# Performance work log

Measured on AMD Instinct MI355X. Metric: run time of the kernel, lower is better.

The kernel has to match this reference:

```python
import jax, jax.numpy as jnp
import numpy as np

N_NODES = 50000
N_EDGES = 500000
D_IN = 128
D_HID = 128
D_OUT = 128
N_GRAPHS = 1024


def gcn_conv(x, W, b, row, col, n_nodes):
    # x: [N, d_in] -> [N, d_out]; PyG GCNConv with add_self_loops + symmetric norm
    h = x @ W  # [N, d_out]
    loops = jnp.arange(n_nodes, dtype=row.dtype)
    r = jnp.concatenate([row, loops])  # source
    c = jnp.concatenate([col, loops])  # target
    deg = jax.ops.segment_sum(jnp.ones(r.shape[0], dtype=x.dtype), c, num_segments=n_nodes)
    dinv = jnp.where(deg > 0, jax.lax.rsqrt(jnp.maximum(deg, 1.0)), 0.0)
    norm = dinv[r] * dinv[c]  # [E+N]
    msg = h[r] * norm[:, None]  # gather + scale
    out = jax.ops.segment_sum(msg, c, num_segments=n_nodes)  # scatter-add at targets
    return out + b


def setup_inputs() -> dict:
    key = jax.random.key(0)
    ks = jax.random.split(key, 10)
    x = jax.random.normal(ks[0], (N_NODES, D_IN), dtype=jnp.float32)
    edge_index = jax.random.randint(ks[1], (2, N_EDGES), 0, N_NODES, dtype=jnp.int64)
    batch = jnp.sort(jax.random.randint(ks[2], (N_NODES,), 0, N_GRAPHS, dtype=jnp.int64))
    s1 = 1.0 / np.sqrt(D_IN)
    s2 = 1.0 / np.sqrt(D_HID)
    W1 = jax.random.uniform(ks[3], (D_IN, D_HID), jnp.float32, -s1, s1)
    b1 = jnp.zeros((D_HID,), jnp.float32)
    W2 = jax.random.uniform(ks[4], (D_HID, D_HID), jnp.float32, -s2, s2)
    b2 = jnp.zeros((D_HID,), jnp.float32)
    Wf = jax.random.uniform(ks[5], (D_HID, D_OUT), jnp.float32, -s2, s2)
    bf = jax.random.uniform(ks[6], (D_OUT,), jnp.float32, -s2, s2)
    return {"x": x, "edge_index": edge_index, "batch": batch,
            "W1": W1, "b1": b1, "W2": W2, "b2": b2, "Wf": Wf, "bf": bf}


def reference(x, edge_index, batch, W1, b1, W2, b2, Wf, bf):
    n = x.shape[0]
    row, col = edge_index[0], edge_index[1]
    h = jax.nn.relu(gcn_conv(x, W1, b1, row, col, n))
    h = jax.nn.relu(gcn_conv(h, W2, b2, row, col, n))
    # global_mean_pool over graph ids
    sums = jax.ops.segment_sum(h, batch, num_segments=N_GRAPHS)  # [G, d]
    cnts = jax.ops.segment_sum(jnp.ones((n,), h.dtype), batch, num_segments=N_GRAPHS)
    pooled = sums / jnp.maximum(cnts, 1.0)[:, None]
    return pooled @ Wf + bf  # [G, D_OUT]
```

## Files before the change

### kernel.cpp

```cpp
#include <hip/hip_runtime.h>
#include <hip/hip_bf16.h>


#define D 128

typedef __attribute__((ext_vector_type(8))) short short8;
typedef __attribute__((ext_vector_type(4))) float f32x4;

__device__ __forceinline__ int swz(int row, int kbyte) {
    return row * 256 + (kbyte ^ ((row & 7) << 4));
}

__global__ void k_zero(int4* __restrict__ p, int n4) {
    int i = blockIdx.x * blockDim.x + threadIdx.x;
    if (i < n4) p[i] = make_int4(0, 0, 0, 0);
}

__global__ void k_deg(const int* __restrict__ col, int* __restrict__ cnt, int E) {
    int e = blockIdx.x * blockDim.x + threadIdx.x;
    if (e < E) atomicAdd(&cnt[col[e]], 1);
}

__global__ __launch_bounds__(256) void k_scan_partial(const int* __restrict__ cnt,
                                                      int* __restrict__ partial, int n) {
    int t = threadIdx.x;
    int base = blockIdx.x * 1024 + t * 4;
    int s = 0;
#pragma unroll
    for (int j = 0; j < 4; ++j) {
        int i = base + j;
        if (i < n) s += cnt[i];
    }
#pragma unroll
    for (int o = 32; o > 0; o >>= 1) s += __shfl_down(s, o, 64);
    __shared__ int ws[4];
    if ((t & 63) == 0) ws[t >> 6] = s;
    __syncthreads();
    if (t == 0) partial[blockIdx.x] = ws[0] + ws[1] + ws[2] + ws[3];
}

__global__ void k_scan_mid(int* __restrict__ partial, int nb,
                           int* __restrict__ offs, int n) {
    if (threadIdx.x == 0 && blockIdx.x == 0) {
        int run = 0;
        for (int i = 0; i < nb; ++i) { int v = partial[i]; partial[i] = run; run += v; }
        offs[n] = run;
    }
}

__global__ __launch_bounds__(256) void k_scan_final(const int* __restrict__ cnt,
                                                    const int* __restrict__ pprefix,
                                                    int* __restrict__ offs,
                                                    int* __restrict__ cursor,
                                                    float* __restrict__ dinv, int n) {
    int t = threadIdx.x;
    int lane = t & 63;
    int base = blockIdx.x * 1024 + t * 4;
    int v[4];
    int s = 0;
#pragma unroll
    for (int j = 0; j < 4; ++j) {
        int i = base + j;
        v[j] = (i < n) ? cnt[i] : 0;
        s += v[j];
    }
    int inc = s;
#pragma unroll
    for (int o = 1; o < 64; o <<= 1) {
        int u = __shfl_up(inc, o, 64);
        if (lane >= o) inc += u;
    }
    __shared__ int wsum[4];
    if (lane == 63) wsum[t >> 6] = inc;
    __syncthreads();
    int woff = 0;
    int w = t >> 6;
    for (int k = 0; k < w; ++k) woff += wsum[k];
    int excl = woff + (inc - s) + pprefix[blockIdx.x];
#pragma unroll
    for (int j = 0; j < 4; ++j) {
        int i = base + j;
        if (i < n) {
            offs[i] = excl;
            cursor[i] = excl;
            dinv[i] = 1.0f / sqrtf((float)(v[j] + 1));
        }
        excl += v[j];
    }
}

__global__ void k_fill(const int* __restrict__ ei, int* __restrict__ cursor,
                       int* __restrict__ csr, int E) {
    int e = blockIdx.x * blockDim.x + threadIdx.x;
    if (e < E) {
        int r = ei[e];
        int c = ei[E + e];
        int pos = atomicAdd(&cursor[c], 1);
        csr[pos] = r;
    }
}

__global__ __launch_bounds__(256) void k_wcvt(const float* __restrict__ W1,
                                              const float* __restrict__ W2,
                                              ushort* __restrict__ h1, ushort* __restrict__ l1,
                                              ushort* __restrict__ h2, ushort* __restrict__ l2) {
    int b = blockIdx.x;
    const float* W = (b < 8) ? W1 : W2;
    ushort* Wh = (b < 8) ? h1 : h2;
    ushort* Wl = (b < 8) ? l1 : l2;
    int t = (b & 7) * 256 + threadIdx.x;
    int nrow = t >> 4;
    int kc = t & 15;
    uint hw[8], lw[8];
#pragma unroll
    for (int j = 0; j < 8; ++j) {
        float f = W[(kc * 8 + j) * D + nrow];
        uint ub = __float_as_uint(f);
        uint hb = ub & 0xffff0000u;
        float r = f - __uint_as_float(hb);
        hw[j] = hb >> 16;
        lw[j] = __float_as_uint(r) >> 16;
    }
    uint4 vh = make_uint4(hw[0] | (hw[1] << 16), hw[2] | (hw[3] << 16),
                          hw[4] | (hw[5] << 16), hw[6] | (hw[7] << 16));
    uint4 vl = make_uint4(lw[0] | (lw[1] << 16), lw[2] | (lw[3] << 16),
                          lw[4] | (lw[5] << 16), lw[6] | (lw[7] << 16));
    *(uint4*)&Wh[nrow * D + kc * 8] = vh;
    *(uint4*)&Wl[nrow * D + kc * 8] = vl;
}

#define TM 64
template <bool ASLICED>
__global__ __launch_bounds__(256) void k_gemm(const float* __restrict__ A,
                                              const ushort* __restrict__ Bt_hi,
                                              const ushort* __restrict__ Bt_lo,
                                              const float* __restrict__ dinv,
                                              float* __restrict__ C, int n) {
    extern __shared__ char lds[];
    char* Bh = lds;
    char* Bl = lds + 32 * 1024;

    int tid = threadIdx.x;
    int wave = tid >> 6, lane = tid & 63;
    int li = lane & 15, lg = lane >> 4;
    int row0 = blockIdx.x * TM;
    int grow = row0 + wave * 16 + li;
    bool valid = grow < n;

    float4 a[4][2];
#pragma unroll
    for (int ks = 0; ks < 4; ++ks) {
        int k0 = ks * 32 + lg * 8;
        if (valid) {
            const float4* p;
            if (ASLICED)
                p = (const float4*)(A + ((size_t)(k0 >> 4) * n + grow) * 16 + (k0 & 15));
            else
                p = (const float4*)(A + (size_t)grow * D + k0);
            a[ks][0] = p[0];
            a[ks][1] = p[1];
        } else {
            a[ks][0] = make_float4(0.f, 0.f, 0.f, 0.f);
            a[ks][1] = make_float4(0.f, 0.f, 0.f, 0.f);
        }
    }

#pragma unroll
    for (int it = tid; it < 2048; it += 256) {
        int r = it >> 4, kc = it & 15;
        uint4 vh = *(const uint4*)(Bt_hi + r * D + kc * 8);
        uint4 vl = *(const uint4*)(Bt_lo + r * D + kc * 8);
        *(uint4*)(Bh + swz(r, kc * 16)) = vh;
        *(uint4*)(Bl + swz(r, kc * 16)) = vl;
    }
    __syncthreads();

    short8 ah[4], al[4];
#pragma unroll
    for (int ks = 0; ks < 4; ++ks) {
        float f[8] = {a[ks][0].x, a[ks][0].y, a[ks][0].z, a[ks][0].w,
                      a[ks][1].x, a[ks][1].y, a[ks][1].z, a[ks][1].w};
#pragma unroll
        for (int j = 0; j < 8; ++j) {
            uint ub = __float_as_uint(f[j]);
            uint hb = ub & 0xffff0000u;
            float r = f[j] - __uint_as_float(hb);
            ah[ks][j] = (short)(hb >> 16);
            al[ks][j] = (short)(__float_as_uint(r) >> 16);
        }
    }

    f32x4 acc[8];
#pragma unroll
    for (int i = 0; i < 8; ++i) acc[i] = (f32x4){0.f, 0.f, 0.f, 0.f};

#pragma unroll
    for (int ks = 0; ks < 4; ++ks) {
        int kb = ks * 64 + lg * 16;
#pragma unroll
        for (int nt = 0; nt < 8; ++nt) {
            short8 bh = *(const short8*)(Bh + swz(nt * 16 + li, kb));
            short8 bl = *(const short8*)(Bl + swz(nt * 16 + li, kb));
            acc[nt] = __builtin_amdgcn_mfma_f32_16x16x32_bf16(ah[ks], bh, acc[nt], 0, 0, 0);
            acc[nt] = __builtin_amdgcn_mfma_f32_16x16x32_bf16(al[ks], bh, acc[nt], 0, 0, 0);
            acc[nt] = __builtin_amdgcn_mfma_f32_16x16x32_bf16(ah[ks], bl, acc[nt], 0, 0, 0);
        }
    }

    int crow0 = row0 + wave * 16 + lg * 4;
#pragma unroll
    for (int j = 0; j < 4; ++j) {
        int gr = crow0 + j;
        if (gr < n) {
            float dv = dinv[gr];
#pragma unroll
            for (int nt = 0; nt < 8; ++nt)
                C[((size_t)nt * n + gr) * 16 + li] = acc[nt][j] * dv;
        }
    }
}

#define AGG_NB 64
__global__ __launch_bounds__(256) void k_agg(const float* __restrict__ hs,
                                             const float* __restrict__ dinv,
                                             const int* __restrict__ offs,
                                             const int* __restrict__ csr,
                                             const float* __restrict__ bias,
                                             float* __restrict__ outs, int n) {
    int slice = blockIdx.x & 7;
    int chunk = blockIdx.x >> 3;
    int node = chunk * AGG_NB + (threadIdx.x >> 2);
    if (node >= n) return;
    int l4 = (threadIdx.x & 3) * 4;

    const float* hbase = hs + (size_t)slice * n * 16;
    float di = dinv[node];
    int s = offs[node], e = offs[node + 1];
    f32x4 acc = *(const f32x4*)(hbase + (size_t)node * 16 + l4);
    int p = s;
    for (; p + 8 <= e; p += 8) {
        int r0 = csr[p],     r1 = csr[p + 1], r2 = csr[p + 2], r3 = csr[p + 3];
        int r4 = csr[p + 4], r5 = csr[p + 5], r6 = csr[p + 6], r7 = csr[p + 7];
        f32x4 h0 = *(const f32x4*)(hbase + (size_t)r0 * 16 + l4);
        f32x4 h1 = *(const f32x4*)(hbase + (size_t)r1 * 16 + l4);
        f32x4 h2 = *(const f32x4*)(hbase + (size_t)r2 * 16 + l4);
        f32x4 h3 = *(const f32x4*)(hbase + (size_t)r3 * 16 + l4);
        f32x4 h4 = *(const f32x4*)(hbase + (size_t)r4 * 16 + l4);
        f32x4 h5 = *(const f32x4*)(hbase + (size_t)r5 * 16 + l4);
        f32x4 h6 = *(const f32x4*)(hbase + (size_t)r6 * 16 + l4);
        f32x4 h7 = *(const f32x4*)(hbase + (size_t)r7 * 16 + l4);
        acc += ((h0 + h1) + (h2 + h3)) + ((h4 + h5) + (h6 + h7));
    }
    for (; p + 4 <= e; p += 4) {
        int r0 = csr[p], r1 = csr[p + 1], r2 = csr[p + 2], r3 = csr[p + 3];
        f32x4 h0 = *(const f32x4*)(hbase + (size_t)r0 * 16 + l4);
        f32x4 h1 = *(const f32x4*)(hbase + (size_t)r1 * 16 + l4);
        f32x4 h2 = *(const f32x4*)(hbase + (size_t)r2 * 16 + l4);
        f32x4 h3 = *(const f32x4*)(hbase + (size_t)r3 * 16 + l4);
        acc += (h0 + h1) + (h2 + h3);
    }
    for (; p < e; ++p) {
        int r = csr[p];
        acc += *(const f32x4*)(hbase + (size_t)r * 16 + l4);
    }
    f32x4 b4 = *(const f32x4*)(bias + slice * 16 + l4);
    f32x4 v;
#pragma unroll
    for (int j = 0; j < 4; ++j) v[j] = fmaxf(acc[j] * di + b4[j], 0.f);
    __builtin_nontemporal_store(v, (f32x4*)(outs + ((size_t)slice * n + node) * 16 + l4));
}

__global__ __launch_bounds__(128) void k_poolfinal(const float* __restrict__ hs,
                                                   const int* __restrict__ batch, int n,
                                                   const float* __restrict__ Wf,
                                                   const float* __restrict__ bf,
                                                   float* __restrict__ out) {
    int g = blockIdx.x;
    int lo = 0, hi = n;
    while (lo < hi) { int m = (lo + hi) >> 1; if (batch[m] < g) lo = m + 1; else hi = m; }
    int s = lo;
    lo = s; hi = n;
    while (lo < hi) { int m = (lo + hi) >> 1; if (batch[m] < g + 1) lo = m + 1; else hi = m; }
    int e = lo;

    int d = threadIdx.x;
    const float* base = hs + (size_t)(d >> 4) * n * 16 + (d & 15);
    float a0 = 0.f, a1 = 0.f, a2 = 0.f, a3 = 0.f;
    int i = s;
    for (; i + 4 <= e; i += 4) {
        a0 += base[(size_t)i * 16];
        a1 += base[(size_t)(i + 1) * 16];
        a2 += base[(size_t)(i + 2) * 16];
        a3 += base[(size_t)(i + 3) * 16];
    }
    for (; i < e; ++i) a0 += base[(size_t)i * 16];
    float acc = (a0 + a1) + (a2 + a3);
    float cnt = (float)(e - s);
    if (cnt < 1.f) cnt = 1.f;

    __shared__ float pr[D];
    pr[d] = acc / cnt;
    __syncthreads();
    float o = bf[d];
#pragma unroll 8
    for (int k = 0; k < D; ++k) o += pr[k] * Wf[k * D + d];
    out[g * D + d] = o;
}

extern "C" void kernel_launch(void* const* d_in, const int* in_sizes, int n_in,
                              void* d_out, int out_size, void* d_ws, size_t ws_size,
                              hipStream_t stream) {
    const float* x  = (const float*)d_in[0];
    const int*   ei = (const int*)d_in[1];
    const int*   bt = (const int*)d_in[2];
    const float* W1 = (const float*)d_in[3];
    const float* b1 = (const float*)d_in[4];
    const float* W2 = (const float*)d_in[5];
    const float* b2 = (const float*)d_in[6];
    const float* Wf = (const float*)d_in[7];
    const float* bf = (const float*)d_in[8];
    float* out = (float*)d_out;

    int n = in_sizes[2];
    int E = in_sizes[1] / 2;
    int G = out_size / D;

    char* w = (char*)d_ws;
    size_t off = 0;
    auto alloc = [&](size_t bytes) -> void* {
        void* p = w + off;
        off = (off + bytes + 511) & ~(size_t)511;
        return p;
    };
    int*    degcnt = (int*)alloc((size_t)n * 4);
    int*    cursor = (int*)alloc((size_t)n * 4);
    int*    offs   = (int*)alloc((size_t)(n + 1) * 4);
    float*  dinv   = (float*)alloc((size_t)n * 4);
    int*    csr    = (int*)alloc((size_t)E * 4);
    float*  hw     = (float*)alloc((size_t)n * D * 4);
    float*  ha     = (float*)alloc((size_t)n * D * 4);
    int*    partial= (int*)alloc((size_t)256 * 4);
    ushort* wt1h   = (ushort*)alloc((size_t)D * D * 2);
    ushort* wt1l   = (ushort*)alloc((size_t)D * D * 2);
    ushort* wt2h   = (ushort*)alloc((size_t)D * D * 2);
    ushort* wt2l   = (ushort*)alloc((size_t)D * D * 2);

    int n4 = (n + 3) / 4;
    k_zero<<<(n4 + 255) / 256, 256, 0, stream>>>((int4*)degcnt, n4);

    int eb = (E + 255) / 256;
    int sb = (n + 1023) / 1024;
    k_deg<<<eb, 256, 0, stream>>>(ei + E, degcnt, E);
    k_scan_partial<<<sb, 256, 0, stream>>>(degcnt, partial, n);
    k_scan_mid<<<1, 64, 0, stream>>>(partial, sb, offs, n);
    k_scan_final<<<sb, 256, 0, stream>>>(degcnt, partial, offs, cursor, dinv, n);
    k_fill<<<eb, 256, 0, stream>>>(ei, cursor, csr, E);

    k_wcvt<<<16, 256, 0, stream>>>(W1, W2, wt1h, wt1l, wt2h, wt2l);

    int gb = (n + TM - 1) / TM;
    int ab = 8 * ((n + AGG_NB - 1) / AGG_NB);
    size_t lds_bytes = 64 * 1024;

    k_gemm<false><<<gb, 256, lds_bytes, stream>>>(x, wt1h, wt1l, dinv, hw, n);
    k_agg<<<ab, 256, 0, stream>>>(hw, dinv, offs, csr, b1, ha, n);
    k_gemm<true><<<gb, 256, lds_bytes, stream>>>(ha, wt2h, wt2l, dinv, hw, n);
    k_agg<<<ab, 256, 0, stream>>>(hw, dinv, offs, csr, b2, ha, n);
    k_poolfinal<<<G, 128, 0, stream>>>(ha, bt, n, Wf, bf, out);
}
```

Measured before the change: 187.5 us.

## Fuse setup kernels, vectorize edge loops, and enlarge GEMM tiles to 128 rows

Merges the degree-buffer zeroing and weight split-conversion into one init kernel, and folds the single-thread mid-scan into the final scan, where each block sums the preceding partials itself. This cuts the number of launches. The degree and CSR-fill kernels now handle two edges per thread using int2 loads. The GEMM goes from a 64-row tile with 256 threads to a 128-row tile with 512 threads, so the B-matrix LDS staging is amortized over more rows, at the cost of fewer blocks and higher register pressure.

```diff
diff --git a/kernel.cpp b/kernel.cpp
--- a/kernel.cpp
+++ b/kernel.cpp
@@ -11,104 +11,22 @@
     return row * 256 + (kbyte ^ ((row & 7) << 4));
 }
 
-__global__ void k_zero(int4* __restrict__ p, int n4) {
-    int i = blockIdx.x * blockDim.x + threadIdx.x;
-    if (i < n4) p[i] = make_int4(0, 0, 0, 0);
-}
-
-__global__ void k_deg(const int* __restrict__ col, int* __restrict__ cnt, int E) {
-    int e = blockIdx.x * blockDim.x + threadIdx.x;
-    if (e < E) atomicAdd(&cnt[col[e]], 1);
-}
-
-__global__ __launch_bounds__(256) void k_scan_partial(const int* __restrict__ cnt,
-                                                      int* __restrict__ partial, int n) {
-    int t = threadIdx.x;
-    int base = blockIdx.x * 1024 + t * 4;
-    int s = 0;
-#pragma unroll
-    for (int j = 0; j < 4; ++j) {
-        int i = base + j;
-        if (i < n) s += cnt[i];
-    }
-#pragma unroll
-    for (int o = 32; o > 0; o >>= 1) s += __shfl_down(s, o, 64);
-    __shared__ int ws[4];
-    if ((t & 63) == 0) ws[t >> 6] = s;
-    __syncthreads();
-    if (t == 0) partial[blockIdx.x] = ws[0] + ws[1] + ws[2] + ws[3];
-}
-
-__global__ void k_scan_mid(int* __restrict__ partial, int nb,
-                           int* __restrict__ offs, int n) {
-    if (threadIdx.x == 0 && blockIdx.x == 0) {
-        int run = 0;
-        for (int i = 0; i < nb; ++i) { int v = partial[i]; partial[i] = run; run += v; }
-        offs[n] = run;
-    }
-}
-
-__global__ __launch_bounds__(256) void k_scan_final(const int* __restrict__ cnt,
-                                                    const int* __restrict__ pprefix,
-                                                    int* __restrict__ offs,
-                                                    int* __restrict__ cursor,
-                                                    float* __restrict__ dinv, int n) {
-    int t = threadIdx.x;
-    int lane = t & 63;
-    int base = blockIdx.x * 1024 + t * 4;
-    int v[4];
-    int s = 0;
-#pragma unroll
-    for (int j = 0; j < 4; ++j) {
-        int i = base + j;
-        v[j] = (i < n) ? cnt[i] : 0;
-        s += v[j];
-    }
-    int inc = s;
-#pragma unroll
-    for (int o = 1; o < 64; o <<= 1) {
-        int u = __shfl_up(inc, o, 64);
-        if (lane >= o) inc += u;
-    }
-    __shared__ int wsum[4];
-    if (lane == 63) wsum[t >> 6] = inc;
-    __syncthreads();
-    int woff = 0;
-    int w = t >> 6;
-    for (int k = 0; k < w; ++k) woff += wsum[k];
-    int excl = woff + (inc - s) + pprefix[blockIdx.x];
-#pragma unroll
-    for (int j = 0; j < 4; ++j) {
-        int i = base + j;
-        if (i < n) {
-            offs[i] = excl;
-            cursor[i] = excl;
-            dinv[i] = 1.0f / sqrtf((float)(v[j] + 1));
-        }
-        excl += v[j];
-    }
-}
-
-__global__ void k_fill(const int* __restrict__ ei, int* __restrict__ cursor,
-                       int* __restrict__ csr, int E) {
-    int e = blockIdx.x * blockDim.x + threadIdx.x;
-    if (e < E) {
-        int r = ei[e];
-        int c = ei[E + e];
-        int pos = atomicAdd(&cursor[c], 1);
-        csr[pos] = r;
-    }
-}
-
-__global__ __launch_bounds__(256) void k_wcvt(const float* __restrict__ W1,
+__global__ __launch_bounds__(256) void k_init(int4* __restrict__ degcnt4, int n4, int zb,
+                                              const float* __restrict__ W1,
                                               const float* __restrict__ W2,
                                               ushort* __restrict__ h1, ushort* __restrict__ l1,
                                               ushort* __restrict__ h2, ushort* __restrict__ l2) {
     int b = blockIdx.x;
-    const float* W = (b < 8) ? W1 : W2;
-    ushort* Wh = (b < 8) ? h1 : h2;
-    ushort* Wl = (b < 8) ? l1 : l2;
-    int t = (b & 7) * 256 + threadIdx.x;
+    if (b < zb) {
+        int i = b * 256 + threadIdx.x;
+        if (i < n4) degcnt4[i] = make_int4(0, 0, 0, 0);
+        return;
+    }
+    int bb = b - zb;
+    const float* W = (bb < 8) ? W1 : W2;
+    ushort* Wh = (bb < 8) ? h1 : h2;
+    ushort* Wl = (bb < 8) ? l1 : l2;
+    int t = (bb & 7) * 256 + threadIdx.x;
     int nrow = t >> 4;
     int kc = t & 15;
     uint hw[8], lw[8];
@@ -129,13 +47,109 @@
     *(uint4*)&Wl[nrow * D + kc * 8] = vl;
 }
 
-#define TM 64
+__global__ void k_deg(const int* __restrict__ col, int* __restrict__ cnt, int E) {
+    int e = (blockIdx.x * blockDim.x + threadIdx.x) * 2;
+    if (e + 1 < E) {
+        int2 c = *(const int2*)&col[e];
+        atomicAdd(&cnt[c.x], 1);
+        atomicAdd(&cnt[c.y], 1);
+    } else if (e < E) {
+        atomicAdd(&cnt[col[e]], 1);
+    }
+}
+
+__global__ __launch_bounds__(256) void k_scan_partial(const int* __restrict__ cnt,
+                                                      int* __restrict__ partial, int n) {
+    int t = threadIdx.x;
+    int base = blockIdx.x * 1024 + t * 4;
+    int s = 0;
+#pragma unroll
+    for (int j = 0; j < 4; ++j) {
+        int i = base + j;
+        if (i < n) s += cnt[i];
+    }
+#pragma unroll
+    for (int o = 32; o > 0; o >>= 1) s += __shfl_down(s, o, 64);
+    __shared__ int ws[4];
+    if ((t & 63) == 0) ws[t >> 6] = s;
+    __syncthreads();
+    if (t == 0) partial[blockIdx.x] = ws[0] + ws[1] + ws[2] + ws[3];
+}
+
+__global__ __launch_bounds__(256) void k_scan_final(const int* __restrict__ cnt,
+                                                    const int* __restrict__ partial,
+                                                    int* __restrict__ offs,
+                                                    int* __restrict__ cursor,
+                                                    float* __restrict__ dinv,
+                                                    int n, int E) {
+    int t = threadIdx.x;
+    int lane = t & 63;
+    int base = blockIdx.x * 1024 + t * 4;
+    int v[4];
+    int s = 0;
+#pragma unroll
+    for (int j = 0; j < 4; ++j) {
+        int i = base + j;
+        v[j] = (i < n) ? cnt[i] : 0;
+        s += v[j];
+    }
+    int inc = s;
+#pragma unroll
+    for (int o = 1; o < 64; o <<= 1) {
+        int u = __shfl_up(inc, o, 64);
+        if (lane >= o) inc += u;
+    }
+    __shared__ int wsum[4];
+    __shared__ int bpref;
+    if (lane == 63) wsum[t >> 6] = inc;
+    if (t == 0) {
+        int run = 0;
+        for (int b = 0; b < blockIdx.x; ++b) run += partial[b];
+        bpref = run;
+        if (blockIdx.x == 0) offs[n] = E;
+    }
+    __syncthreads();
+    int woff = 0;
+    int w = t >> 6;
+    for (int k = 0; k < w; ++k) woff += wsum[k];
+    int excl = woff + (inc - s) + bpref;
+#pragma unroll
+    for (int j = 0; j < 4; ++j) {
+        int i = base + j;
+        if (i < n) {
+            offs[i] = excl;
+            cursor[i] = excl;
+            dinv[i] = 1.0f / sqrtf((float)(v[j] + 1));
+        }
+        excl += v[j];
+    }
+}
+
+__global__ void k_fill(const int* __restrict__ ei, int* __restrict__ cursor,
+                       int* __restrict__ csr, int E) {
+    int e = (blockIdx.x * blockDim.x + threadIdx.x) * 2;
+    if (e + 1 < E) {
+        int2 r = *(const int2*)&ei[e];
+        int2 c = *(const int2*)&ei[E + e];
+        int p0 = atomicAdd(&cursor[c.x], 1);
+        csr[p0] = r.x;
+        int p1 = atomicAdd(&cursor[c.y], 1);
+        csr[p1] = r.y;
+    } else if (e < E) {
+        int r = ei[e];
+        int c = ei[E + e];
+        int pos = atomicAdd(&cursor[c], 1);
+        csr[pos] = r;
+    }
+}
+
+#define TM 128
 template <bool ASLICED>
-__global__ __launch_bounds__(256) void k_gemm(const float* __restrict__ A,
-                                              const ushort* __restrict__ Bt_hi,
-                                              const ushort* __restrict__ Bt_lo,
-                                              const float* __restrict__ dinv,
-                                              float* __restrict__ C, int n) {
+__global__ __launch_bounds__(512, 4) void k_gemm(const float* __restrict__ A,
+                                                 const ushort* __restrict__ Bt_hi,
+                                                 const ushort* __restrict__ Bt_lo,
+                                                 const float* __restrict__ dinv,
+                                                 float* __restrict__ C, int n) {
     extern __shared__ char lds[];
     char* Bh = lds;
     char* Bl = lds + 32 * 1024;
@@ -166,7 +180,7 @@
     }
 
 #pragma unroll
-    for (int it = tid; it < 2048; it += 256) {
+    for (int it = tid; it < 2048; it += 512) {
         int r = it >> 4, kc = it & 15;
         uint4 vh = *(const uint4*)(Bt_hi + r * D + kc * 8);
         uint4 vl = *(const uint4*)(Bt_lo + r * D + kc * 8);
@@ -346,25 +360,24 @@
     ushort* wt2l   = (ushort*)alloc((size_t)D * D * 2);
 
     int n4 = (n + 3) / 4;
-    k_zero<<<(n4 + 255) / 256, 256, 0, stream>>>((int4*)degcnt, n4);
-
-    int eb = (E + 255) / 256;
+    int zb = (n4 + 255) / 256;
+    k_init<<<zb + 16, 256, 0, stream>>>((int4*)degcnt, n4, zb,
+                                        W1, W2, wt1h, wt1l, wt2h, wt2l);
+
+    int e2b = (E / 2 + 255) / 256 + 1;
     int sb = (n + 1023) / 1024;
-    k_deg<<<eb, 256, 0, stream>>>(ei + E, degcnt, E);
+    k_deg<<<e2b, 256, 0, stream>>>(ei + E, degcnt, E);
     k_scan_partial<<<sb, 256, 0, stream>>>(degcnt, partial, n);
-    k_scan_mid<<<1, 64, 0, stream>>>(partial, sb, offs, n);
-    k_scan_final<<<sb, 256, 0, stream>>>(degcnt, partial, offs, cursor, dinv, n);
-    k_fill<<<eb, 256, 0, stream>>>(ei, cursor, csr, E);
-
-    k_wcvt<<<16, 256, 0, stream>>>(W1, W2, wt1h, wt1l, wt2h, wt2l);
+    k_scan_final<<<sb, 256, 0, stream>>>(degcnt, partial, offs, cursor, dinv, n, E);
+    k_fill<<<e2b, 256, 0, stream>>>(ei, cursor, csr, E);
 
     int gb = (n + TM - 1) / TM;
     int ab = 8 * ((n + AGG_NB - 1) / AGG_NB);
     size_t lds_bytes = 64 * 1024;
 
-    k_gemm<false><<<gb, 256, lds_bytes, stream>>>(x, wt1h, wt1l, dinv, hw, n);
+    k_gemm<false><<<gb, 512, lds_bytes, stream>>>(x, wt1h, wt1l, dinv, hw, n);
     k_agg<<<ab, 256, 0, stream>>>(hw, dinv, offs, csr, b1, ha, n);
-    k_gemm<true><<<gb, 256, lds_bytes, stream>>>(ha, wt2h, wt2l, dinv, hw, n);
+    k_gemm<true><<<gb, 512, lds_bytes, stream>>>(ha, wt2h, wt2l, dinv, hw, n);
     k_agg<<<ab, 256, 0, stream>>>(hw, dinv, offs, csr, b2, ha, n);
     k_poolfinal<<<G, 128, 0, stream>>>(ha, bt, n, Wf, bf, out);
 }
```

Result: faster. 172.9 us (-7.8%).
